# Kernel optimization log

Hardware: AMD Instinct MI355X
Metric: run time of the kernel (lower is better)

Reference implementation:

```python
import jax, jax.numpy as jnp
import numpy as np

HIDDEN = 2048
ENGRAM = 256
ENTRIES = 32768
K = 3  # conv kernel size
LN_EPS = 1e-6
NORM_EPS = 1e-8
INV_TEMP = ENGRAM ** 0.5  # retrieval_temperature = 1/sqrt(engram_dim)
CLAMP_MIN = 0.5  # step 0 < clamp_until_step=800 -> hard clamp active


def _l2norm(x):
    n = jnp.linalg.norm(x, axis=-1, keepdims=True)
    return x / jnp.maximum(n, NORM_EPS)


def _rmsnorm(x, w, eps=LN_EPS):
    ms = jnp.mean(jnp.square(x), axis=-1, keepdims=True)
    return x * jax.lax.rsqrt(ms + eps) * w


def _layernorm(x, g, b, eps=LN_EPS):
    mu = jnp.mean(x, axis=-1, keepdims=True)
    var = jnp.mean(jnp.square(x - mu), axis=-1, keepdims=True)
    return (x - mu) * jax.lax.rsqrt(var + eps) * g + b


def setup_inputs() -> dict:
    key = jax.random.key(0)
    ks = jax.random.split(key, 7)
    s = lambda fan: 1.0 / np.sqrt(fan)
    return {
        "hidden_state": jax.random.normal(ks[0], (4, 1024, HIDDEN), jnp.float32),
        "table": jax.random.normal(ks[1], (ENTRIES, ENGRAM), jnp.float32),
        "Wq": jax.random.normal(ks[2], (HIDDEN, ENGRAM), jnp.float32) * s(HIDDEN),
        "ln_gamma": jnp.ones((ENGRAM,), jnp.float32),
        "ln_beta": jnp.zeros((ENGRAM,), jnp.float32),
        "Wk": jax.random.normal(ks[3], (ENGRAM, HIDDEN), jnp.float32) * s(ENGRAM),
        "Wv": jax.random.normal(ks[4], (ENGRAM, HIDDEN), jnp.float32) * s(ENGRAM),
        "gate_norm_w": jnp.ones((HIDDEN,), jnp.float32),
        "key_norm_w": jnp.ones((HIDDEN,), jnp.float32),
        # depthwise causal conv weight [C, K] (torch init zeros; randn for a meaningful test)
        "conv_w": jax.random.normal(ks[5], (HIDDEN, K), jnp.float32) * 0.1,
    }


def reference(hidden_state, table, Wq, ln_gamma, ln_beta, Wk, Wv,
              gate_norm_w, key_norm_w, conv_w):
    B, L, C = hidden_state.shape
    # --- retrieval: cosine-sim softmax attention over frozen table ---
    q = jnp.einsum('blc,ce->ble', hidden_state, Wq)
    qn = _l2norm(q)
    tn = _l2norm(table)
    sims = jnp.einsum('ble,te->blt', qn, tn)            # [B,L,T]
    weights = jax.nn.softmax(sims * INV_TEMP, axis=-1)
    retrieved = jnp.einsum('blt,te->ble', weights, table)
    retrieved = _layernorm(retrieved, ln_gamma, ln_beta)
    # --- key/value projections + gating ---
    key_ = jnp.einsum('ble,ec->blc', retrieved, Wk)
    value = jnp.einsum('ble,ec->blc', retrieved, Wv)
    h_norm = _rmsnorm(hidden_state, gate_norm_w)
    k_norm = _rmsnorm(key_, key_norm_w)
    dot = jnp.sum(h_norm * k_norm, axis=-1, keepdims=True)
    raw_gate = jax.nn.sigmoid(dot / np.sqrt(C).astype(np.float32))
    gate = jnp.maximum(raw_gate, CLAMP_MIN)             # clamp phase (step < 800)
    gated = gate * value                                 # [B,L,C]
    # --- causal depthwise conv along seq (left pad K-1) ---
    padded = jnp.pad(gated, ((0, 0), (K - 1, 0), (0, 0)))
    conv = sum(conv_w[:, k] * padded[:, k:k + L, :] for k in range(K))
    return jax.nn.silu(conv), gate
```

## Files before the change

kernel.cpp:

```cpp
#include <hip/hip_runtime.h>
#include <stdint.h>


#define NTOK 4096
#define CDIM 2048
#define EDIM 256
#define TROWS 32768
#define SPLIT 16
#define BN 32
#define OUT0 (NTOK * CDIM)

typedef __attribute__((ext_vector_type(8))) short bf16x8;
typedef __attribute__((ext_vector_type(4))) short bf16x4;
typedef __attribute__((ext_vector_type(4))) float f32x4;

__device__ inline float bf2f(unsigned short u) { return __uint_as_float((unsigned)u << 16); }
__device__ inline unsigned short f2bf(float f) {
  unsigned x = __float_as_uint(f);
  x += 0x7fffu + ((x >> 16) & 1u);
  return (unsigned short)(x >> 16);
}
__device__ inline unsigned cvt_pk_bf16(float lo, float hi) {
  unsigned r;
  asm("v_cvt_pk_bf16_f32 %0, %1, %2" : "=v"(r) : "v"(lo), "v"(hi));
  return r;
}
__device__ inline void gll16(const void* g, void* l) {
  __builtin_amdgcn_global_load_lds((const __attribute__((address_space(1))) void*)g,
                                   (__attribute__((address_space(3))) void*)l, 16, 0, 0);
}

__global__ __launch_bounds__(256) void cast_bf16_kernel(
    const float* __restrict__ in, unsigned short* __restrict__ out) {
  const int idx = blockIdx.x * 256 + threadIdx.x;
  float4 v0 = *reinterpret_cast<const float4*>(&in[(size_t)idx * 8]);
  float4 v1 = *reinterpret_cast<const float4*>(&in[(size_t)idx * 8 + 4]);
  bf16x8 o;
  o[0] = (short)f2bf(v0.x); o[1] = (short)f2bf(v0.y);
  o[2] = (short)f2bf(v0.z); o[3] = (short)f2bf(v0.w);
  o[4] = (short)f2bf(v1.x); o[5] = (short)f2bf(v1.y);
  o[6] = (short)f2bf(v1.z); o[7] = (short)f2bf(v1.w);
  *reinterpret_cast<bf16x8*>(&out[(size_t)idx * 8]) = o;
}

__global__ __launch_bounds__(256) void transpose_cast_kernel(
    const float* __restrict__ in, unsigned short* __restrict__ out, int R, int C) {
  __shared__ float lt[32][33];
  const int tid = threadIdx.x;
  const int r0 = blockIdx.x * 32, c0 = blockIdx.y * 32;
  {
    int r = tid >> 3, c4 = (tid & 7) * 4;
    float4 v = *reinterpret_cast<const float4*>(&in[(size_t)(r0 + r) * C + c0 + c4]);
    lt[r][c4] = v.x; lt[r][c4 + 1] = v.y; lt[r][c4 + 2] = v.z; lt[r][c4 + 3] = v.w;
  }
  __syncthreads();
  {
    int c = tid >> 3, r4 = (tid & 7) * 4;
#pragma unroll
    for (int j = 0; j < 4; ++j)
      out[(size_t)(c0 + c) * R + r0 + r4 + j] = f2bf(lt[r4 + j][c]);
  }
}

__global__ __launch_bounds__(256) void tabprep_kernel(
    const float* __restrict__ table, unsigned short* __restrict__ tnb,
    unsigned short* __restrict__ tvb) {
  __shared__ float lt[32][257];
  __shared__ float inv[32];
  const int tid = threadIdx.x, nb = blockIdx.x;
  const int r0 = nb * 32;
#pragma unroll
  for (int i = 0; i < 8; ++i) {
    int id = i * 256 + tid;
    int row = id >> 6, e4 = (id & 63) * 4;
    float4 v = *reinterpret_cast<const float4*>(&table[(size_t)(r0 + row) * EDIM + e4]);
    lt[row][e4] = v.x; lt[row][e4 + 1] = v.y; lt[row][e4 + 2] = v.z; lt[row][e4 + 3] = v.w;
  }
  __syncthreads();
  {
    int row = tid >> 3, sub = tid & 7;
    float ss = 0.f;
#pragma unroll
    for (int j = 0; j < 32; ++j) { float v = lt[row][sub + 8 * j]; ss = fmaf(v, v, ss); }
    ss += __shfl_xor(ss, 1); ss += __shfl_xor(ss, 2); ss += __shfl_xor(ss, 4);
    if (sub == 0) inv[row] = 1.f / fmaxf(sqrtf(ss), 1e-8f);
  }
  __syncthreads();
#pragma unroll
  for (int i = 0; i < 4; ++i) {
    int q = i * 256 + tid;
    {
      int c8 = q >> 5, row = q & 31;
      bf16x8 v;
#pragma unroll
      for (int j = 0; j < 8; ++j) v[j] = (short)f2bf(lt[row][c8 * 8 + j] * inv[row]);
      *reinterpret_cast<bf16x8*>(&tnb[(size_t)nb * 8192 + q * 8]) = v;
    }
    {
      int hi = q >> 8, e = q & 255;
      bf16x8 v;
#pragma unroll
      for (int j = 0; j < 8; ++j) v[j] = (short)f2bf(lt[hi * 8 + j][e]);
      *reinterpret_cast<bf16x8*>(&tvb[(size_t)nb * 8192 + q * 8]) = v;
    }
  }
}

__global__ __launch_bounds__(256, 2) void gemm_bt_kernel(
    const unsigned short* __restrict__ A, const unsigned short* __restrict__ BT,
    unsigned short* __restrict__ C, int M, int N, int K) {
  __shared__ alignas(16) unsigned short sA[2][128 * 64];
  __shared__ alignas(16) unsigned short sB[2][128 * 64];
  const int tid = threadIdx.x;
  const int lane = tid & 63;
  const int wave = tid >> 6;
  const int laneLo = lane & 15, laneHi = lane >> 4;
  const int nbn = N >> 7;
  const int bm = blockIdx.x / nbn, bn = blockIdx.x % nbn;
  const int wr = wave >> 1, wc = wave & 1;
  f32x4 acc[4][4];
#pragma unroll
  for (int m = 0; m < 4; ++m)
#pragma unroll
    for (int n = 0; n < 4; ++n) acc[m][n] = (f32x4){0.f, 0.f, 0.f, 0.f};
  const int nkt = K >> 6;
  auto STAGE = [&](int b, int kt) {
#pragma unroll
    for (int i = 0; i < 4; ++i) {
      int q = i * 256 + tid;
      int row = q >> 3, cl = q & 7;
      int cs = cl ^ (row & 7);
      gll16(A + ((size_t)(bm * 128 + row) * K + kt * 64 + cs * 8), &sA[b][q * 8]);
      gll16(BT + ((size_t)(bn * 128 + row) * K + kt * 64 + cs * 8), &sB[b][q * 8]);
    }
  };
  STAGE(0, 0);
  for (int kt = 0; kt < nkt; ++kt) {
    __syncthreads();
    if (kt + 1 < nkt) STAGE((kt & 1) ^ 1, kt + 1);
    const unsigned short* pA = sA[kt & 1];
    const unsigned short* pB = sB[kt & 1];
#pragma unroll
    for (int ks = 0; ks < 2; ++ks) {
      bf16x8 af[4], bfr[4];
#pragma unroll
      for (int m = 0; m < 4; ++m) {
        int row = wr * 64 + m * 16 + laneLo;
        af[m] = *reinterpret_cast<const bf16x8*>(&pA[(row * 8 + ((ks * 4 + laneHi) ^ (row & 7))) * 8]);
      }
#pragma unroll
      for (int n = 0; n < 4; ++n) {
        int row = wc * 64 + n * 16 + laneLo;
        bfr[n] = *reinterpret_cast<const bf16x8*>(&pB[(row * 8 + ((ks * 4 + laneHi) ^ (row & 7))) * 8]);
      }
#pragma unroll
      for (int m = 0; m < 4; ++m)
#pragma unroll
        for (int n = 0; n < 4; ++n)
          acc[m][n] = __builtin_amdgcn_mfma_f32_16x16x32_bf16(af[m], bfr[n], acc[m][n], 0, 0, 0);
    }
  }
#pragma unroll
  for (int m = 0; m < 4; ++m)
#pragma unroll
    for (int n = 0; n < 4; ++n)
#pragma unroll
      for (int r = 0; r < 4; ++r)
        C[(size_t)(bm * 128 + wr * 64 + m * 16 + laneHi * 4 + r) * N +
          bn * 128 + wc * 64 + n * 16 + laneLo] = f2bf(acc[m][n][r]);
}

__global__ __launch_bounds__(64) void normq_kernel(
    const unsigned short* __restrict__ qb, unsigned short* __restrict__ qn) {
  const int r = blockIdx.x, lane = threadIdx.x;
  bf16x4 v = *reinterpret_cast<const bf16x4*>(&qb[(size_t)r * EDIM + lane * 4]);
  float f0 = bf2f((unsigned short)v[0]), f1 = bf2f((unsigned short)v[1]);
  float f2 = bf2f((unsigned short)v[2]), f3 = bf2f((unsigned short)v[3]);
  float ss = f0 * f0 + f1 * f1 + f2 * f2 + f3 * f3;
#pragma unroll
  for (int m = 1; m <= 32; m <<= 1) ss += __shfl_xor(ss, m);
  const float inv = 1.f / fmaxf(sqrtf(ss), 1e-8f);
  bf16x4 o;
  o[0] = (short)f2bf(f0 * inv); o[1] = (short)f2bf(f1 * inv);
  o[2] = (short)f2bf(f2 * inv); o[3] = (short)f2bf(f3 * inv);
  *reinterpret_cast<bf16x4*>(&qn[(size_t)r * EDIM + lane * 4]) = o;
}

__global__ __launch_bounds__(256, 2) void attn_kernel(
    const unsigned short* __restrict__ qn, const unsigned short* __restrict__ tnb,
    const unsigned short* __restrict__ tvb, unsigned short* __restrict__ Opart,
    float* __restrict__ lpart) {
  __shared__ alignas(16) unsigned short bufK[2][32 * 256];
  __shared__ alignas(16) unsigned short bufV[2][32 * 256];
  __shared__ alignas(16) unsigned short pbuf[4][2][4][16][8];
  const int tid = threadIdx.x;
  const int wave = tid >> 6, lane = tid & 63;
  const int laneLo = lane & 15, laneHi = lane >> 4;
  const int split = blockIdx.y;
  const int tokBase = blockIdx.x * 128 + wave * 32;
  bf16x8 qf[2][8];
#pragma unroll
  for (int g = 0; g < 2; ++g)
#pragma unroll
    for (int ks = 0; ks < 8; ++ks)
      qf[g][ks] = *reinterpret_cast<const bf16x8*>(
          qn + (size_t)(tokBase + g * 16 + laneLo) * EDIM + ks * 32 + laneHi * 8);
  f32x4 o[2][16];
#pragma unroll
  for (int g = 0; g < 2; ++g)
#pragma unroll
    for (int f = 0; f < 16; ++f) o[g][f] = (f32x4){0.f, 0.f, 0.f, 0.f};
  float l_run[2] = {0.f, 0.f};
  const int nt = (TROWS / SPLIT) / BN;
  const int nb0 = split * nt;
  {
    const unsigned short* sk = tnb + (size_t)nb0 * 8192;
    const unsigned short* sv = tvb + (size_t)nb0 * 8192;
#pragma unroll
    for (int i = 0; i < 4; ++i) {
      gll16(sk + (i * 256 + tid) * 8, &bufK[0][(i * 256 + tid) * 8]);
      gll16(sv + (i * 256 + tid) * 8, &bufV[0][(i * 256 + tid) * 8]);
    }
  }
  for (int it = 0; it < nt; ++it) {
    __syncthreads();
    const int cur = it & 1;
    if (it + 1 < nt) {
      const unsigned short* sk = tnb + (size_t)(nb0 + it + 1) * 8192;
      const unsigned short* sv = tvb + (size_t)(nb0 + it + 1) * 8192;
#pragma unroll
      for (int i = 0; i < 4; ++i) {
        gll16(sk + (i * 256 + tid) * 8, &bufK[cur ^ 1][(i * 256 + tid) * 8]);
        gll16(sv + (i * 256 + tid) * 8, &bufV[cur ^ 1][(i * 256 + tid) * 8]);
      }
    }
    f32x4 z00 = {0.f, 0.f, 0.f, 0.f}, z01 = z00, z10 = z00, z11 = z00;
#pragma unroll
    for (int ks = 0; ks < 8; ++ks) {
      const int c8 = ks * 4 + laneHi;
      bf16x8 a0 = *reinterpret_cast<const bf16x8*>(&bufK[cur][(c8 * 32 + laneLo) * 8]);
      bf16x8 a1 = *reinterpret_cast<const bf16x8*>(&bufK[cur][(c8 * 32 + 16 + laneLo) * 8]);
      z00 = __builtin_amdgcn_mfma_f32_16x16x32_bf16(a0, qf[0][ks], z00, 0, 0, 0);
      z01 = __builtin_amdgcn_mfma_f32_16x16x32_bf16(a1, qf[0][ks], z01, 0, 0, 0);
      z10 = __builtin_amdgcn_mfma_f32_16x16x32_bf16(a0, qf[1][ks], z10, 0, 0, 0);
      z11 = __builtin_amdgcn_mfma_f32_16x16x32_bf16(a1, qf[1][ks], z11, 0, 0, 0);
    }
#pragma unroll
    for (int g = 0; g < 2; ++g) {
      const f32x4 za = g ? z10 : z00;
      const f32x4 zb = g ? z11 : z01;
      float p[8];
#pragma unroll
      for (int r = 0; r < 4; ++r) {
        p[r] = __expf(fmaf(16.f, za[r], -16.f));
        p[4 + r] = __expf(fmaf(16.f, zb[r], -16.f));
      }
      l_run[g] += ((p[0] + p[1]) + (p[2] + p[3])) + ((p[4] + p[5]) + (p[6] + p[7]));
      const int hi2 = laneHi >> 1, j0 = (laneHi & 1) * 4;
      *reinterpret_cast<uint2*>(&pbuf[wave][g][hi2][laneLo][j0]) =
          make_uint2(cvt_pk_bf16(p[0], p[1]), cvt_pk_bf16(p[2], p[3]));
      *reinterpret_cast<uint2*>(&pbuf[wave][g][2 + hi2][laneLo][j0]) =
          make_uint2(cvt_pk_bf16(p[4], p[5]), cvt_pk_bf16(p[6], p[7]));
    }
    asm volatile("s_waitcnt lgkmcnt(0)" ::: "memory");
    __builtin_amdgcn_sched_barrier(0);
    bf16x8 pa0 = *reinterpret_cast<const bf16x8*>(&pbuf[wave][0][laneHi][laneLo][0]);
    bf16x8 pa1 = *reinterpret_cast<const bf16x8*>(&pbuf[wave][1][laneHi][laneLo][0]);
#pragma unroll
    for (int f = 0; f < 16; ++f) {
      bf16x8 vb = *reinterpret_cast<const bf16x8*>(
          &bufV[cur][(laneHi * 256 + f * 16 + laneLo) * 8]);
      o[0][f] = __builtin_amdgcn_mfma_f32_16x16x32_bf16(pa0, vb, o[0][f], 0, 0, 0);
      o[1][f] = __builtin_amdgcn_mfma_f32_16x16x32_bf16(pa1, vb, o[1][f], 0, 0, 0);
    }
  }
#pragma unroll
  for (int g = 0; g < 2; ++g) {
    float l = l_run[g];
    l += __shfl_xor(l, 16);
    l += __shfl_xor(l, 32);
    if (lane < 16) lpart[(size_t)split * NTOK + tokBase + g * 16 + laneLo] = l;
#pragma unroll
    for (int f = 0; f < 16; ++f)
#pragma unroll
      for (int r = 0; r < 4; ++r)
        Opart[((size_t)split * NTOK + tokBase + g * 16 + laneHi * 4 + r) * EDIM +
              f * 16 + laneLo] = f2bf(o[g][f][r]);
  }
}

__global__ __launch_bounds__(256) void combine_ln_kernel(
    const unsigned short* __restrict__ Opart, const float* __restrict__ lpart,
    const float* __restrict__ gamma, const float* __restrict__ beta,
    unsigned short* __restrict__ retr) {
  __shared__ float red[4][2];
  const int t = blockIdx.x, e = threadIdx.x;
  const int wave = e >> 6, lane = e & 63;
  float acc = 0.f, l = 0.f;
#pragma unroll
  for (int s = 0; s < SPLIT; ++s) {
    acc += bf2f(Opart[((size_t)s * NTOK + t) * EDIM + e]);
    l += lpart[(size_t)s * NTOK + t];
  }
  const float r = acc / l;
  float s1 = r, s2 = r * r;
#pragma unroll
  for (int m = 1; m <= 32; m <<= 1) { s1 += __shfl_xor(s1, m); s2 += __shfl_xor(s2, m); }
  if (lane == 0) { red[wave][0] = s1; red[wave][1] = s2; }
  __syncthreads();
  s1 = red[0][0] + red[1][0] + red[2][0] + red[3][0];
  s2 = red[0][1] + red[1][1] + red[2][1] + red[3][1];
  const float mu = s1 * (1.f / 256.f);
  const float var = s2 * (1.f / 256.f) - mu * mu;
  const float rs = rsqrtf(var + 1e-6f);
  retr[(size_t)t * EDIM + e] = f2bf((r - mu) * rs * gamma[e] + beta[e]);
}

__global__ __launch_bounds__(256) void gate_kernel(
    const float* __restrict__ hidden, const unsigned short* __restrict__ kv,
    const float* __restrict__ gw, const float* __restrict__ kwn,
    unsigned short* __restrict__ gatedb, float* __restrict__ gate_out) {
  __shared__ float red[4][3];
  const int t = blockIdx.x, tid = threadIdx.x;
  const int wave = tid >> 6, lane = tid & 63;
  float vv[8];
  float ssh = 0.f, ssk = 0.f, shk = 0.f;
#pragma unroll
  for (int i = 0; i < 8; ++i) {
    int cc = tid + i * 256;
    float h = hidden[(size_t)t * CDIM + cc];
    float k = bf2f(kv[(size_t)t * 4096 + cc]);
    vv[i] = bf2f(kv[(size_t)t * 4096 + 2048 + cc]);
    ssh = fmaf(h, h, ssh);
    ssk = fmaf(k, k, ssk);
    shk = fmaf(h * gw[cc], k * kwn[cc], shk);
  }
#pragma unroll
  for (int m = 1; m <= 32; m <<= 1) {
    ssh += __shfl_xor(ssh, m); ssk += __shfl_xor(ssk, m); shk += __shfl_xor(shk, m);
  }
  if (lane == 0) { red[wave][0] = ssh; red[wave][1] = ssk; red[wave][2] = shk; }
  __syncthreads();
  ssh = red[0][0] + red[1][0] + red[2][0] + red[3][0];
  ssk = red[0][1] + red[1][1] + red[2][1] + red[3][1];
  shk = red[0][2] + red[1][2] + red[2][2] + red[3][2];
  const float rsh = rsqrtf(ssh * (1.f / 2048.f) + 1e-6f);
  const float rsk = rsqrtf(ssk * (1.f / 2048.f) + 1e-6f);
  const float dot = rsh * rsk * shk;
  const float rg = 1.f / (1.f + __expf(-dot * 0.02209708691207961f));
  const float gate = fmaxf(rg, 0.5f);
  if (tid == 0) gate_out[t] = gate;
#pragma unroll
  for (int i = 0; i < 8; ++i) {
    int cc = tid + i * 256;
    gatedb[(size_t)t * CDIM + cc] = f2bf(gate * vv[i]);
  }
}

__global__ __launch_bounds__(256) void conv_kernel(
    const unsigned short* __restrict__ gatedb, const float* __restrict__ convw,
    float* __restrict__ out0) {
  const int t = blockIdx.x, tid = threadIdx.x;
  const int l = t & 1023;
  const int c0 = tid * 8;
  bf16x8 gz;
#pragma unroll
  for (int j = 0; j < 8; ++j) gz[j] = 0;
  bf16x8 g2 = *reinterpret_cast<const bf16x8*>(gatedb + (size_t)t * CDIM + c0);
  bf16x8 g1 = (l >= 1) ? *reinterpret_cast<const bf16x8*>(gatedb + (size_t)(t - 1) * CDIM + c0) : gz;
  bf16x8 g0 = (l >= 2) ? *reinterpret_cast<const bf16x8*>(gatedb + (size_t)(t - 2) * CDIM + c0) : gz;
  float res[8];
#pragma unroll
  for (int j = 0; j < 8; ++j) {
    int c = c0 + j;
    float x = convw[c * 3 + 0] * bf2f((unsigned short)g0[j])
            + convw[c * 3 + 1] * bf2f((unsigned short)g1[j])
            + convw[c * 3 + 2] * bf2f((unsigned short)g2[j]);
    res[j] = x / (1.f + __expf(-x));
  }
  *reinterpret_cast<float4*>(out0 + (size_t)t * CDIM + c0) =
      make_float4(res[0], res[1], res[2], res[3]);
  *reinterpret_cast<float4*>(out0 + (size_t)t * CDIM + c0 + 4) =
      make_float4(res[4], res[5], res[6], res[7]);
}

extern "C" void kernel_launch(void* const* d_in, const int* in_sizes, int n_in,
                              void* d_out, int out_size, void* d_ws, size_t ws_size,
                              hipStream_t stream) {
  const float* hidden = (const float*)d_in[0];
  const float* table  = (const float*)d_in[1];
  const float* Wq     = (const float*)d_in[2];
  const float* ln_g   = (const float*)d_in[3];
  const float* ln_b   = (const float*)d_in[4];
  const float* Wk     = (const float*)d_in[5];
  const float* Wv     = (const float*)d_in[6];
  const float* gnw    = (const float*)d_in[7];
  const float* knw    = (const float*)d_in[8];
  const float* convw  = (const float*)d_in[9];
  float* out = (float*)d_out;

  char* w = (char*)d_ws;
  const size_t MB = 1u << 20;
  unsigned short* hb     = (unsigned short*)(w);
  unsigned short* qb     = (unsigned short*)(w + 16 * MB);
  unsigned short* Opart  = (unsigned short*)(w);
  unsigned short* gatedb = (unsigned short*)(w);
  unsigned short* qn     = (unsigned short*)(w + 32 * MB);
  unsigned short* retr   = (unsigned short*)(w + 32 * MB);
  unsigned short* WkvT   = (unsigned short*)(w + 34 * MB);
  unsigned short* WqT    = (unsigned short*)(w + 36 * MB);
  float*          lpart  = (float*)(w + 37 * MB);
  unsigned short* tnb    = (unsigned short*)(w + 38 * MB);
  unsigned short* tvb    = (unsigned short*)(w + 54 * MB);
  unsigned short* kv     = (unsigned short*)(w + 38 * MB);

  cast_bf16_kernel<<<NTOK * CDIM / 2048, 256, 0, stream>>>(hidden, hb);
  transpose_cast_kernel<<<dim3(64, 8), 256, 0, stream>>>(Wq, WqT, CDIM, EDIM);
  transpose_cast_kernel<<<dim3(8, 64), 256, 0, stream>>>(Wk, WkvT, EDIM, CDIM);
  transpose_cast_kernel<<<dim3(8, 64), 256, 0, stream>>>(Wv, WkvT + (size_t)CDIM * EDIM, EDIM, CDIM);
  tabprep_kernel<<<TROWS / 32, 256, 0, stream>>>(table, tnb, tvb);
  gemm_bt_kernel<<<(NTOK / 128) * (EDIM / 128), 256, 0, stream>>>(hb, WqT, qb, NTOK, EDIM, CDIM);
  normq_kernel<<<NTOK, 64, 0, stream>>>(qb, qn);
  attn_kernel<<<dim3(NTOK / 128, SPLIT), 256, 0, stream>>>(qn, tnb, tvb, Opart, lpart);
  combine_ln_kernel<<<NTOK, 256, 0, stream>>>(Opart, lpart, ln_g, ln_b, retr);
  gemm_bt_kernel<<<(NTOK / 128) * (2 * CDIM / 128), 256, 0, stream>>>(retr, WkvT, kv, NTOK, 2 * CDIM, EDIM);
  gate_kernel<<<NTOK, 256, 0, stream>>>(hidden, kv, gnw, knw, gatedb, out + OUT0);
  conv_kernel<<<NTOK, 256, 0, stream>>>(gatedb, convw, out);
}
```

Measured before the change: 245.7 us.

## Enlarge attention blocks to 256 tokens, split-K the Q projection, merge transposes

The attention kernel now runs 512 threads per block covering 256 tokens, so each staged table tile is reused by twice as many queries. Probabilities are shared through LDS and the PV step is split across waves by token group and feature slice. Blocks are remapped with a swizzled grid, and MFMA sections get raised wave priority. The Q projection GEMM is split along K into two fp32 partials that a new kernel sums and L2-normalizes, which doubles the parallelism of that small GEMM. The Wk/Wv transposes are merged into one launch, at the cost of an extra barrier per iteration and heavier register use in attention.

```diff
diff --git a/kernel.cpp b/kernel.cpp
--- a/kernel.cpp
+++ b/kernel.cpp
@@ -7,11 +7,9 @@
 #define EDIM 256
 #define TROWS 32768
 #define SPLIT 16
-#define BN 32
 #define OUT0 (NTOK * CDIM)
 
 typedef __attribute__((ext_vector_type(8))) short bf16x8;
-typedef __attribute__((ext_vector_type(4))) short bf16x4;
 typedef __attribute__((ext_vector_type(4))) float f32x4;
 
 __device__ inline float bf2f(unsigned short u) { return __uint_as_float((unsigned)u << 16); }
@@ -44,10 +42,13 @@
 }
 
 __global__ __launch_bounds__(256) void transpose_cast_kernel(
-    const float* __restrict__ in, unsigned short* __restrict__ out, int R, int C) {
+    const float* __restrict__ in0, const float* __restrict__ in1,
+    unsigned short* __restrict__ out, int R, int C) {
   __shared__ float lt[32][33];
   const int tid = threadIdx.x;
   const int r0 = blockIdx.x * 32, c0 = blockIdx.y * 32;
+  const float* in = blockIdx.z ? in1 : in0;
+  unsigned short* op = out + (size_t)blockIdx.z * R * C;
   {
     int r = tid >> 3, c4 = (tid & 7) * 4;
     float4 v = *reinterpret_cast<const float4*>(&in[(size_t)(r0 + r) * C + c0 + c4]);
@@ -58,7 +59,7 @@
     int c = tid >> 3, r4 = (tid & 7) * 4;
 #pragma unroll
     for (int j = 0; j < 4; ++j)
-      out[(size_t)(c0 + c) * R + r0 + r4 + j] = f2bf(lt[r4 + j][c]);
+      op[(size_t)(c0 + c) * R + r0 + r4 + j] = f2bf(lt[r4 + j][c]);
   }
 }
 
@@ -106,9 +107,10 @@
   }
 }
 
+template <bool F32OUT>
 __global__ __launch_bounds__(256, 2) void gemm_bt_kernel(
     const unsigned short* __restrict__ A, const unsigned short* __restrict__ BT,
-    unsigned short* __restrict__ C, int M, int N, int K) {
+    void* __restrict__ Cout, int M, int N, int Kfull, int klen) {
   __shared__ alignas(16) unsigned short sA[2][128 * 64];
   __shared__ alignas(16) unsigned short sB[2][128 * 64];
   const int tid = threadIdx.x;
@@ -117,21 +119,22 @@
   const int laneLo = lane & 15, laneHi = lane >> 4;
   const int nbn = N >> 7;
   const int bm = blockIdx.x / nbn, bn = blockIdx.x % nbn;
+  const int koff = blockIdx.y * klen;
   const int wr = wave >> 1, wc = wave & 1;
   f32x4 acc[4][4];
 #pragma unroll
   for (int m = 0; m < 4; ++m)
 #pragma unroll
     for (int n = 0; n < 4; ++n) acc[m][n] = (f32x4){0.f, 0.f, 0.f, 0.f};
-  const int nkt = K >> 6;
+  const int nkt = klen >> 6;
   auto STAGE = [&](int b, int kt) {
 #pragma unroll
     for (int i = 0; i < 4; ++i) {
       int q = i * 256 + tid;
       int row = q >> 3, cl = q & 7;
       int cs = cl ^ (row & 7);
-      gll16(A + ((size_t)(bm * 128 + row) * K + kt * 64 + cs * 8), &sA[b][q * 8]);
-      gll16(BT + ((size_t)(bn * 128 + row) * K + kt * 64 + cs * 8), &sB[b][q * 8]);
+      gll16(A + ((size_t)(bm * 128 + row) * Kfull + koff + kt * 64 + cs * 8), &sA[b][q * 8]);
+      gll16(BT + ((size_t)(bn * 128 + row) * Kfull + koff + kt * 64 + cs * 8), &sB[b][q * 8]);
     }
   };
   STAGE(0, 0);
@@ -165,86 +168,82 @@
 #pragma unroll
     for (int n = 0; n < 4; ++n)
 #pragma unroll
-      for (int r = 0; r < 4; ++r)
-        C[(size_t)(bm * 128 + wr * 64 + m * 16 + laneHi * 4 + r) * N +
-          bn * 128 + wc * 64 + n * 16 + laneLo] = f2bf(acc[m][n][r]);
-}
-
-__global__ __launch_bounds__(64) void normq_kernel(
-    const unsigned short* __restrict__ qb, unsigned short* __restrict__ qn) {
-  const int r = blockIdx.x, lane = threadIdx.x;
-  bf16x4 v = *reinterpret_cast<const bf16x4*>(&qb[(size_t)r * EDIM + lane * 4]);
-  float f0 = bf2f((unsigned short)v[0]), f1 = bf2f((unsigned short)v[1]);
-  float f2 = bf2f((unsigned short)v[2]), f3 = bf2f((unsigned short)v[3]);
-  float ss = f0 * f0 + f1 * f1 + f2 * f2 + f3 * f3;
+      for (int r = 0; r < 4; ++r) {
+        size_t idx = (size_t)(bm * 128 + wr * 64 + m * 16 + laneHi * 4 + r) * N +
+                     bn * 128 + wc * 64 + n * 16 + laneLo;
+        if (F32OUT)
+          ((float*)Cout)[(size_t)blockIdx.y * M * N + idx] = acc[m][n][r];
+        else
+          ((unsigned short*)Cout)[idx] = f2bf(acc[m][n][r]);
+      }
+}
+
+__global__ __launch_bounds__(256) void qcombine_kernel(
+    const float* __restrict__ qpart, unsigned short* __restrict__ qn) {
+  __shared__ float red[4];
+  const int t = blockIdx.x, e = threadIdx.x;
+  const int wave = e >> 6, lane = e & 63;
+  float v = qpart[(size_t)t * EDIM + e] + qpart[((size_t)NTOK + t) * EDIM + e];
+  float ss = v * v;
 #pragma unroll
   for (int m = 1; m <= 32; m <<= 1) ss += __shfl_xor(ss, m);
+  if (lane == 0) red[wave] = ss;
+  __syncthreads();
+  ss = red[0] + red[1] + red[2] + red[3];
   const float inv = 1.f / fmaxf(sqrtf(ss), 1e-8f);
-  bf16x4 o;
-  o[0] = (short)f2bf(f0 * inv); o[1] = (short)f2bf(f1 * inv);
-  o[2] = (short)f2bf(f2 * inv); o[3] = (short)f2bf(f3 * inv);
-  *reinterpret_cast<bf16x4*>(&qn[(size_t)r * EDIM + lane * 4]) = o;
-}
-
-__global__ __launch_bounds__(256, 2) void attn_kernel(
+  qn[(size_t)t * EDIM + e] = f2bf(v * inv);
+}
+
+__global__ __launch_bounds__(512, 2) void attn_kernel(
     const unsigned short* __restrict__ qn, const unsigned short* __restrict__ tnb,
     const unsigned short* __restrict__ tvb, unsigned short* __restrict__ Opart,
     float* __restrict__ lpart) {
-  __shared__ alignas(16) unsigned short bufK[2][32 * 256];
-  __shared__ alignas(16) unsigned short bufV[2][32 * 256];
-  __shared__ alignas(16) unsigned short pbuf[4][2][4][16][8];
+  __shared__ alignas(16) unsigned short bufK[2][8192];
+  __shared__ alignas(16) unsigned short bufV[2][8192];
+  __shared__ alignas(16) unsigned short pbuf[16][16][40];
   const int tid = threadIdx.x;
   const int wave = tid >> 6, lane = tid & 63;
-  const int laneLo = lane & 15, laneHi = lane >> 4;
-  const int split = blockIdx.y;
-  const int tokBase = blockIdx.x * 128 + wave * 32;
+  const int Lo = lane & 15, Hi = lane >> 4;
+  const int cid = (blockIdx.x & 7) * 32 + (blockIdx.x >> 3);
+  const int split = cid >> 4, tb = cid & 15;
+  const int qkBase = tb * 256 + wave * 32;
   bf16x8 qf[2][8];
 #pragma unroll
   for (int g = 0; g < 2; ++g)
 #pragma unroll
     for (int ks = 0; ks < 8; ++ks)
       qf[g][ks] = *reinterpret_cast<const bf16x8*>(
-          qn + (size_t)(tokBase + g * 16 + laneLo) * EDIM + ks * 32 + laneHi * 8);
-  f32x4 o[2][16];
-#pragma unroll
-  for (int g = 0; g < 2; ++g)
-#pragma unroll
-    for (int f = 0; f < 16; ++f) o[g][f] = (f32x4){0.f, 0.f, 0.f, 0.f};
+          qn + (size_t)(qkBase + g * 16 + Lo) * EDIM + ks * 32 + Hi * 8);
+  const int pvG = (wave & 3) * 4;
+  const int pvF = (wave >> 2) * 8;
+  f32x4 o[4][8];
+#pragma unroll
+  for (int ng = 0; ng < 4; ++ng)
+#pragma unroll
+    for (int f = 0; f < 8; ++f) o[ng][f] = (f32x4){0.f, 0.f, 0.f, 0.f};
   float l_run[2] = {0.f, 0.f};
-  const int nt = (TROWS / SPLIT) / BN;
+  const int nt = (TROWS / SPLIT) / 32;
   const int nb0 = split * nt;
-  {
-    const unsigned short* sk = tnb + (size_t)nb0 * 8192;
-    const unsigned short* sv = tvb + (size_t)nb0 * 8192;
-#pragma unroll
-    for (int i = 0; i < 4; ++i) {
-      gll16(sk + (i * 256 + tid) * 8, &bufK[0][(i * 256 + tid) * 8]);
-      gll16(sv + (i * 256 + tid) * 8, &bufV[0][(i * 256 + tid) * 8]);
-    }
+#pragma unroll
+  for (int i = 0; i < 2; ++i) {
+    gll16(tnb + (size_t)nb0 * 8192 + (i * 512 + tid) * 8, &bufK[0][(i * 512 + tid) * 8]);
+    gll16(tvb + (size_t)nb0 * 8192 + (i * 512 + tid) * 8, &bufV[0][(i * 512 + tid) * 8]);
   }
   for (int it = 0; it < nt; ++it) {
+    const int cur = it & 1;
     __syncthreads();
-    const int cur = it & 1;
-    if (it + 1 < nt) {
-      const unsigned short* sk = tnb + (size_t)(nb0 + it + 1) * 8192;
-      const unsigned short* sv = tvb + (size_t)(nb0 + it + 1) * 8192;
-#pragma unroll
-      for (int i = 0; i < 4; ++i) {
-        gll16(sk + (i * 256 + tid) * 8, &bufK[cur ^ 1][(i * 256 + tid) * 8]);
-        gll16(sv + (i * 256 + tid) * 8, &bufV[cur ^ 1][(i * 256 + tid) * 8]);
-      }
-    }
     f32x4 z00 = {0.f, 0.f, 0.f, 0.f}, z01 = z00, z10 = z00, z11 = z00;
+    __builtin_amdgcn_s_setprio(1);
 #pragma unroll
     for (int ks = 0; ks < 8; ++ks) {
-      const int c8 = ks * 4 + laneHi;
-      bf16x8 a0 = *reinterpret_cast<const bf16x8*>(&bufK[cur][(c8 * 32 + laneLo) * 8]);
-      bf16x8 a1 = *reinterpret_cast<const bf16x8*>(&bufK[cur][(c8 * 32 + 16 + laneLo) * 8]);
+      bf16x8 a0 = *reinterpret_cast<const bf16x8*>(&bufK[cur][((ks * 4 + Hi) * 32 + Lo) * 8]);
+      bf16x8 a1 = *reinterpret_cast<const bf16x8*>(&bufK[cur][((ks * 4 + Hi) * 32 + 16 + Lo) * 8]);
       z00 = __builtin_amdgcn_mfma_f32_16x16x32_bf16(a0, qf[0][ks], z00, 0, 0, 0);
       z01 = __builtin_amdgcn_mfma_f32_16x16x32_bf16(a1, qf[0][ks], z01, 0, 0, 0);
       z10 = __builtin_amdgcn_mfma_f32_16x16x32_bf16(a0, qf[1][ks], z10, 0, 0, 0);
       z11 = __builtin_amdgcn_mfma_f32_16x16x32_bf16(a1, qf[1][ks], z11, 0, 0, 0);
     }
+    __builtin_amdgcn_s_setprio(0);
 #pragma unroll
     for (int g = 0; g < 2; ++g) {
       const f32x4 za = g ? z10 : z00;
@@ -256,37 +255,55 @@
         p[4 + r] = __expf(fmaf(16.f, zb[r], -16.f));
       }
       l_run[g] += ((p[0] + p[1]) + (p[2] + p[3])) + ((p[4] + p[5]) + (p[6] + p[7]));
-      const int hi2 = laneHi >> 1, j0 = (laneHi & 1) * 4;
-      *reinterpret_cast<uint2*>(&pbuf[wave][g][hi2][laneLo][j0]) =
+      unsigned short* pb = &pbuf[wave * 2 + g][Lo][0];
+      *reinterpret_cast<uint2*>(pb + Hi * 4) =
           make_uint2(cvt_pk_bf16(p[0], p[1]), cvt_pk_bf16(p[2], p[3]));
-      *reinterpret_cast<uint2*>(&pbuf[wave][g][2 + hi2][laneLo][j0]) =
+      *reinterpret_cast<uint2*>(pb + 16 + Hi * 4) =
           make_uint2(cvt_pk_bf16(p[4], p[5]), cvt_pk_bf16(p[6], p[7]));
     }
-    asm volatile("s_waitcnt lgkmcnt(0)" ::: "memory");
-    __builtin_amdgcn_sched_barrier(0);
-    bf16x8 pa0 = *reinterpret_cast<const bf16x8*>(&pbuf[wave][0][laneHi][laneLo][0]);
-    bf16x8 pa1 = *reinterpret_cast<const bf16x8*>(&pbuf[wave][1][laneHi][laneLo][0]);
-#pragma unroll
-    for (int f = 0; f < 16; ++f) {
+    __syncthreads();
+    if (it + 1 < nt) {
+#pragma unroll
+      for (int i = 0; i < 2; ++i) {
+        gll16(tnb + (size_t)(nb0 + it + 1) * 8192 + (i * 512 + tid) * 8,
+              &bufK[cur ^ 1][(i * 512 + tid) * 8]);
+        gll16(tvb + (size_t)(nb0 + it + 1) * 8192 + (i * 512 + tid) * 8,
+              &bufV[cur ^ 1][(i * 512 + tid) * 8]);
+      }
+    }
+    bf16x8 pa0 = *reinterpret_cast<const bf16x8*>(&pbuf[pvG + 0][Lo][Hi * 8]);
+    bf16x8 pa1 = *reinterpret_cast<const bf16x8*>(&pbuf[pvG + 1][Lo][Hi * 8]);
+    bf16x8 pa2 = *reinterpret_cast<const bf16x8*>(&pbuf[pvG + 2][Lo][Hi * 8]);
+    bf16x8 pa3 = *reinterpret_cast<const bf16x8*>(&pbuf[pvG + 3][Lo][Hi * 8]);
+    __builtin_amdgcn_s_setprio(1);
+#pragma unroll
+    for (int f = 0; f < 8; ++f) {
       bf16x8 vb = *reinterpret_cast<const bf16x8*>(
-          &bufV[cur][(laneHi * 256 + f * 16 + laneLo) * 8]);
+          &bufV[cur][(Hi * 256 + (pvF + f) * 16 + Lo) * 8]);
       o[0][f] = __builtin_amdgcn_mfma_f32_16x16x32_bf16(pa0, vb, o[0][f], 0, 0, 0);
       o[1][f] = __builtin_amdgcn_mfma_f32_16x16x32_bf16(pa1, vb, o[1][f], 0, 0, 0);
-    }
+      o[2][f] = __builtin_amdgcn_mfma_f32_16x16x32_bf16(pa2, vb, o[2][f], 0, 0, 0);
+      o[3][f] = __builtin_amdgcn_mfma_f32_16x16x32_bf16(pa3, vb, o[3][f], 0, 0, 0);
+    }
+    __builtin_amdgcn_s_setprio(0);
   }
 #pragma unroll
   for (int g = 0; g < 2; ++g) {
     float l = l_run[g];
     l += __shfl_xor(l, 16);
     l += __shfl_xor(l, 32);
-    if (lane < 16) lpart[(size_t)split * NTOK + tokBase + g * 16 + laneLo] = l;
-#pragma unroll
-    for (int f = 0; f < 16; ++f)
-#pragma unroll
-      for (int r = 0; r < 4; ++r)
-        Opart[((size_t)split * NTOK + tokBase + g * 16 + laneHi * 4 + r) * EDIM +
-              f * 16 + laneLo] = f2bf(o[g][f][r]);
-  }
+    if (lane < 16) lpart[(size_t)split * NTOK + qkBase + g * 16 + Lo] = l;
+  }
+#pragma unroll
+  for (int ng = 0; ng < 4; ++ng)
+#pragma unroll
+    for (int f = 0; f < 8; ++f)
+#pragma unroll
+      for (int r = 0; r < 4; ++r) {
+        int token = tb * 256 + (pvG + ng) * 16 + Hi * 4 + r;
+        Opart[((size_t)split * NTOK + token) * EDIM + (pvF + f) * 16 + Lo] =
+            f2bf(o[ng][f][r]);
+      }
 }
 
 __global__ __launch_bounds__(256) void combine_ln_kernel(
@@ -401,29 +418,30 @@
 
   char* w = (char*)d_ws;
   const size_t MB = 1u << 20;
-  unsigned short* hb     = (unsigned short*)(w);
-  unsigned short* qb     = (unsigned short*)(w + 16 * MB);
-  unsigned short* Opart  = (unsigned short*)(w);
-  unsigned short* gatedb = (unsigned short*)(w);
+  unsigned short* tnb    = (unsigned short*)(w);
+  unsigned short* tvb    = (unsigned short*)(w + 16 * MB);
+  unsigned short* kv     = (unsigned short*)(w);
   unsigned short* qn     = (unsigned short*)(w + 32 * MB);
   unsigned short* retr   = (unsigned short*)(w + 32 * MB);
   unsigned short* WkvT   = (unsigned short*)(w + 34 * MB);
-  unsigned short* WqT    = (unsigned short*)(w + 36 * MB);
-  float*          lpart  = (float*)(w + 37 * MB);
-  unsigned short* tnb    = (unsigned short*)(w + 38 * MB);
-  unsigned short* tvb    = (unsigned short*)(w + 54 * MB);
-  unsigned short* kv     = (unsigned short*)(w + 38 * MB);
+  float*          lpart  = (float*)(w + 36 * MB);
+  unsigned short* Opart  = (unsigned short*)(w + 37 * MB);
+  unsigned short* hb     = (unsigned short*)(w + 37 * MB);
+  unsigned short* WqT    = (unsigned short*)(w + 53 * MB);
+  float*          qpart  = (float*)(w + 54 * MB);
+  unsigned short* gatedb = (unsigned short*)(w + 37 * MB);
 
   cast_bf16_kernel<<<NTOK * CDIM / 2048, 256, 0, stream>>>(hidden, hb);
-  transpose_cast_kernel<<<dim3(64, 8), 256, 0, stream>>>(Wq, WqT, CDIM, EDIM);
-  transpose_cast_kernel<<<dim3(8, 64), 256, 0, stream>>>(Wk, WkvT, EDIM, CDIM);
-  transpose_cast_kernel<<<dim3(8, 64), 256, 0, stream>>>(Wv, WkvT + (size_t)CDIM * EDIM, EDIM, CDIM);
+  transpose_cast_kernel<<<dim3(64, 8, 1), 256, 0, stream>>>(Wq, Wq, WqT, CDIM, EDIM);
+  transpose_cast_kernel<<<dim3(8, 64, 2), 256, 0, stream>>>(Wk, Wv, WkvT, EDIM, CDIM);
   tabprep_kernel<<<TROWS / 32, 256, 0, stream>>>(table, tnb, tvb);
-  gemm_bt_kernel<<<(NTOK / 128) * (EDIM / 128), 256, 0, stream>>>(hb, WqT, qb, NTOK, EDIM, CDIM);
-  normq_kernel<<<NTOK, 64, 0, stream>>>(qb, qn);
-  attn_kernel<<<dim3(NTOK / 128, SPLIT), 256, 0, stream>>>(qn, tnb, tvb, Opart, lpart);
+  gemm_bt_kernel<true><<<dim3((NTOK / 128) * (EDIM / 128), 2), 256, 0, stream>>>(
+      hb, WqT, qpart, NTOK, EDIM, CDIM, 1024);
+  qcombine_kernel<<<NTOK, 256, 0, stream>>>(qpart, qn);
+  attn_kernel<<<16 * SPLIT, 512, 0, stream>>>(qn, tnb, tvb, Opart, lpart);
   combine_ln_kernel<<<NTOK, 256, 0, stream>>>(Opart, lpart, ln_g, ln_b, retr);
-  gemm_bt_kernel<<<(NTOK / 128) * (2 * CDIM / 128), 256, 0, stream>>>(retr, WkvT, kv, NTOK, 2 * CDIM, EDIM);
+  gemm_bt_kernel<false><<<dim3((NTOK / 128) * (2 * CDIM / 128), 1), 256, 0, stream>>>(
+      retr, WkvT, kv, NTOK, 2 * CDIM, EDIM, EDIM);
   gate_kernel<<<NTOK, 256, 0, stream>>>(hidden, kv, gnw, knw, gatedb, out + OUT0);
   conv_kernel<<<NTOK, 256, 0, stream>>>(gatedb, convw, out);
 }
```

Result: faster. 230.0 us (-6.4%).
